# Performance work log

Hardware: AMD Instinct MI355X
Metric: run time of the kernel (lower is better)

Reference implementation:

```python
import jax, jax.numpy as jnp
import numpy as np

B, K, D = 64, 2048, 32400  # batch, num bases, in_features**2 (180*180)


def setup_inputs() -> dict:
    key = jax.random.key(0)
    k1, k2, k3, k4, k5, k6 = jax.random.split(key, 6)
    s = 1.0 / np.sqrt(K)  # matches uniform(-sqrt(1/K), sqrt(1/K)) scale of weight init
    return {
        "X_re": jax.random.normal(k1, (B, D), dtype=jnp.float32),
        "X_im": jax.random.normal(k2, (B, D), dtype=jnp.float32),
        "bases_re": jax.random.normal(k3, (K, D), dtype=jnp.float32) * 0.004,
        "bases_im": jax.random.normal(k4, (K, D), dtype=jnp.float32) * 0.004,
        "weight_re": jax.random.normal(k5, (K,), dtype=jnp.float32) * s,
        "weight_im": jax.random.normal(k6, (K,), dtype=jnp.float32) * s,
    }


def reference(X_re, X_im, bases_re, bases_im, weight_re, weight_im):
    # Assemble complex64 operands
    X = jax.lax.complex(X_re, X_im)          # [B, D]
    bases = jax.lax.complex(bases_re, bases_im)  # [K, D]
    w = jax.lax.complex(weight_re, weight_im)    # [K]
    # X @ conj(bases)^T -> [B, K]; diag_embed(weight) matmul == per-basis scale
    coeffs = jnp.matmul(X, jnp.conj(bases).T) * w[None, :]
    # project back: [B, K] @ [K, D] -> [B, D]
    out = jnp.matmul(coeffs, bases)
    # complex->channels->complex round trip in the original is the identity
    return out
```

## Files before the change

kernel.cpp:

```cpp
#include <hip/hip_runtime.h>
#include <hip/hip_bf16.h>
#include <cstdint>
#include <cstddef>

#define B_DIM 64
#define K_DIM 2048
#define D_DIM 32400

typedef __bf16 bf16x8 __attribute__((ext_vector_type(8)));
typedef float f32x4 __attribute__((ext_vector_type(4)));

union U128 { uint4 u; bf16x8 b; };

__device__ inline bf16x8 asbf(uint4 u) { U128 x; x.u = u; return x.b; }

__device__ inline uint4 neg4(uint4 u) {
    u.x ^= 0x80008000u; u.y ^= 0x80008000u; u.z ^= 0x80008000u; u.w ^= 0x80008000u;
    return u;
}

__device__ inline f32x4 mfma16(bf16x8 a, bf16x8 b, f32x4 c) {
    return __builtin_amdgcn_mfma_f32_16x16x32_bf16(a, b, c, 0, 0, 0);
}

__device__ inline f32x4 ld4g(const float* __restrict__ p, int d, int dlim) {
    f32x4 r;
    if (d + 4 <= dlim) {
        float4 v = *reinterpret_cast<const float4*>(p + d);
        r[0] = v.x; r[1] = v.y; r[2] = v.z; r[3] = v.w;
    } else {
        #pragma unroll
        for (int j = 0; j < 4; ++j) r[j] = (d + j < dlim) ? p[d + j] : 0.0f;
    }
    return r;
}

__device__ inline uint32_t pk(float a, float b) {
    union { __bf16 h[2]; uint32_t u; } x;
    x.h[0] = (__bf16)a; x.h[1] = (__bf16)b;
    return x.u;
}

#define P1_STRIDE 72

__global__ __launch_bounds__(256) void p1_coeffs(
    const float* __restrict__ Xre, const float* __restrict__ Xim,
    const float* __restrict__ Bre, const float* __restrict__ Bim,
    const float* __restrict__ Wre, const float* __restrict__ Wim,
    float* __restrict__ Cre, float* __restrict__ Cim)
{
    __shared__ __align__(16) __bf16 sX[2][64][P1_STRIDE];
    __shared__ __align__(16) __bf16 sB[2][64][P1_STRIDE];

    const int kt = blockIdx.x;
    const int dc = blockIdx.y;
    const int tid  = threadIdx.x;
    const int lane = tid & 63;
    const int w    = tid >> 6;
    const int r    = lane & 15;
    const int g    = lane >> 4;

    const int kbase  = kt * 64;
    const int dstart = dc * 1024;
    const int dend   = min(dstart + 1024, D_DIM);
    const int nsteps = (dend - dstart + 63) >> 6;

    const int srow = tid >> 4;
    const int sd   = (tid & 15) * 4;

    f32x4 st[16];

    auto LOADS = [&](int s) {
        const int dg = dstart + s * 64 + sd;
        #pragma unroll
        for (int j = 0; j < 4; ++j) {
            const int row = j * 16 + srow;
            st[j]      = ld4g(Xre + (size_t)row * D_DIM, dg, dend);
            st[4 + j]  = ld4g(Xim + (size_t)row * D_DIM, dg, dend);
            st[8 + j]  = ld4g(Bre + (size_t)(kbase + row) * D_DIM, dg, dend);
            st[12 + j] = ld4g(Bim + (size_t)(kbase + row) * D_DIM, dg, dend);
        }
    };

    auto WRITE = [&]() {
        #pragma unroll
        for (int j = 0; j < 4; ++j) {
            const int row = j * 16 + srow;
            *(uint2*)&sX[0][row][sd] = make_uint2(pk(st[j][0],      st[j][1]),      pk(st[j][2],      st[j][3]));
            *(uint2*)&sX[1][row][sd] = make_uint2(pk(st[4 + j][0],  st[4 + j][1]),  pk(st[4 + j][2],  st[4 + j][3]));
            *(uint2*)&sB[0][row][sd] = make_uint2(pk(st[8 + j][0],  st[8 + j][1]),  pk(st[8 + j][2],  st[8 + j][3]));
            *(uint2*)&sB[1][row][sd] = make_uint2(pk(st[12 + j][0], st[12 + j][1]), pk(st[12 + j][2], st[12 + j][3]));
        }
    };

    const int m0  = (w & 1) * 32;
    const int nl0 = (w >> 1) * 32;

    f32x4 accRe[2][2] = {};
    f32x4 accIm[2][2] = {};

    auto COMPUTE = [&]() {
        #pragma unroll
        for (int kk = 0; kk < 2; ++kk) {
            const int dp = kk * 32 + g * 8;
            uint4 xre[2], xim[2], bre[2], bim[2];
            #pragma unroll
            for (int ms = 0; ms < 2; ++ms) {
                xre[ms] = *(const uint4*)&sX[0][m0 + ms * 16 + r][dp];
                xim[ms] = *(const uint4*)&sX[1][m0 + ms * 16 + r][dp];
            }
            #pragma unroll
            for (int ns = 0; ns < 2; ++ns) {
                bre[ns] = *(const uint4*)&sB[0][nl0 + ns * 16 + r][dp];
                bim[ns] = *(const uint4*)&sB[1][nl0 + ns * 16 + r][dp];
            }
            #pragma unroll
            for (int ms = 0; ms < 2; ++ms)
            #pragma unroll
            for (int ns = 0; ns < 2; ++ns) {
                accRe[ms][ns] = mfma16(asbf(xre[ms]), asbf(bre[ns]), accRe[ms][ns]);
                accRe[ms][ns] = mfma16(asbf(xim[ms]), asbf(bim[ns]), accRe[ms][ns]);
                accIm[ms][ns] = mfma16(asbf(xim[ms]), asbf(bre[ns]), accIm[ms][ns]);
                accIm[ms][ns] = mfma16(asbf(neg4(xre[ms])), asbf(bim[ns]), accIm[ms][ns]);
            }
        }
    };

    LOADS(0); WRITE(); __syncthreads();
    for (int s = 0; s < nsteps; ++s) {
        if (s + 1 < nsteps) LOADS(s + 1);
        COMPUTE();
        if (s + 1 < nsteps) {
            __syncthreads();
            WRITE();
            __syncthreads();
        }
    }

    #pragma unroll
    for (int ms = 0; ms < 2; ++ms)
    #pragma unroll
    for (int ns = 0; ns < 2; ++ns) {
        const int kb = kbase + nl0 + ns * 16 + r;
        const float wre = Wre[kb], wim = Wim[kb];
        #pragma unroll
        for (int i = 0; i < 4; ++i) {
            const int b = m0 + ms * 16 + g * 4 + i;
            const float cre = accRe[ms][ns][i];
            const float cim = accIm[ms][ns][i];
            atomicAdd(&Cre[b * K_DIM + kb], cre * wre - cim * wim);
            atomicAdd(&Cim[b * K_DIM + kb], cre * wim + cim * wre);
        }
    }
}

__global__ __launch_bounds__(256) void cbf_kernel(
    const float* __restrict__ Cre, const float* __restrict__ Cim,
    __bf16* __restrict__ CreBf, __bf16* __restrict__ CimBf)
{
    const int i = blockIdx.x * 256 + threadIdx.x;
    if (i < B_DIM * K_DIM) {
        CreBf[i] = (__bf16)Cre[i];
        CimBf[i] = (__bf16)Cim[i];
    }
}

#define P2_STRIDE 72

template <bool WIM>
__global__ __launch_bounds__(256) void p2_project(
    const float* __restrict__ Bre, const float* __restrict__ Bim,
    const __bf16* __restrict__ CreBf, const __bf16* __restrict__ CimBf,
    float* __restrict__ out)
{
    __shared__ __align__(16) __bf16 sT[2][2][64][P2_STRIDE];

    const int dt = blockIdx.x;
    const int kh = blockIdx.y;
    const int d0 = dt * 64;
    const int khbase = kh * (K_DIM / 2);
    const int tid  = threadIdx.x;
    const int lane = tid & 63;
    const int w    = tid >> 6;
    const int r    = lane & 15;
    const int g    = lane >> 4;

    const int kq = tid >> 4;
    const int ds = (tid & 15) * 4;

    f32x4 st[8];

    auto LOADS = [&](int t) {
        const int k0 = khbase + t * 64;
        #pragma unroll
        for (int j = 0; j < 4; ++j) {
            const size_t ro = (size_t)(k0 + kq * 4 + j) * D_DIM;
            st[j]     = ld4g(Bre + ro, d0 + ds, D_DIM);
            st[4 + j] = ld4g(Bim + ro, d0 + ds, D_DIM);
        }
    };

    auto WRITE = [&](int buf) {
        #pragma unroll
        for (int i = 0; i < 4; ++i) {
            *(uint2*)&sT[buf][0][ds + i][kq * 4] =
                make_uint2(pk(st[0][i], st[1][i]), pk(st[2][i], st[3][i]));
            *(uint2*)&sT[buf][1][ds + i][kq * 4] =
                make_uint2(pk(st[4][i], st[5][i]), pk(st[6][i], st[7][i]));
        }
    };

    const int m0  = (w & 1) * 32;
    const int nl0 = (w >> 1) * 32;

    f32x4 accRe[2][2] = {};
    f32x4 accIm[2][2] = {};

    auto COMPUTE = [&](int t, int buf) {
        const int k0 = khbase + t * 64;
        uint4 aRe[2][2], aIm[2][2];
        #pragma unroll
        for (int ms = 0; ms < 2; ++ms) {
            const size_t rowo = (size_t)(m0 + ms * 16 + r) * K_DIM;
            #pragma unroll
            for (int kk = 0; kk < 2; ++kk) {
                aRe[ms][kk] = *(const uint4*)&CreBf[rowo + k0 + kk * 32 + g * 8];
                aIm[ms][kk] = *(const uint4*)&CimBf[rowo + k0 + kk * 32 + g * 8];
            }
        }
        #pragma unroll
        for (int kk = 0; kk < 2; ++kk) {
            uint4 bre[2], bim[2];
            #pragma unroll
            for (int ns = 0; ns < 2; ++ns) {
                bre[ns] = *(const uint4*)&sT[buf][0][nl0 + ns * 16 + r][kk * 32 + g * 8];
                bim[ns] = *(const uint4*)&sT[buf][1][nl0 + ns * 16 + r][kk * 32 + g * 8];
            }
            #pragma unroll
            for (int ms = 0; ms < 2; ++ms)
            #pragma unroll
            for (int ns = 0; ns < 2; ++ns) {
                accRe[ms][ns] = mfma16(asbf(aRe[ms][kk]), asbf(bre[ns]), accRe[ms][ns]);
                accRe[ms][ns] = mfma16(asbf(neg4(aIm[ms][kk])), asbf(bim[ns]), accRe[ms][ns]);
                if (WIM) {
                    accIm[ms][ns] = mfma16(asbf(aRe[ms][kk]), asbf(bim[ns]), accIm[ms][ns]);
                    accIm[ms][ns] = mfma16(asbf(aIm[ms][kk]), asbf(bre[ns]), accIm[ms][ns]);
                }
            }
        }
    };

    const int NT = (K_DIM / 2) / 64;
    LOADS(0); WRITE(0); __syncthreads();
    for (int t = 0; t < NT; ++t) {
        if (t + 1 < NT) LOADS(t + 1);
        COMPUTE(t, t & 1);
        if (t + 1 < NT) WRITE((t + 1) & 1);
        __syncthreads();
    }

    #pragma unroll
    for (int ms = 0; ms < 2; ++ms)
    #pragma unroll
    for (int ns = 0; ns < 2; ++ns) {
        const int d = d0 + nl0 + ns * 16 + r;
        if (d < D_DIM) {
            #pragma unroll
            for (int i = 0; i < 4; ++i) {
                const int b = m0 + ms * 16 + g * 4 + i;
                if (!WIM) {
                    atomicAdd(&out[(size_t)b * D_DIM + d], accRe[ms][ns][i]);
                } else {
                    atomicAdd(&out[((size_t)b * D_DIM + d) * 2],     accRe[ms][ns][i]);
                    atomicAdd(&out[((size_t)b * D_DIM + d) * 2 + 1], accIm[ms][ns][i]);
                }
            }
        }
    }
}

extern "C" void kernel_launch(void* const* d_in, const int* in_sizes, int n_in,
                              void* d_out, int out_size, void* d_ws, size_t ws_size,
                              hipStream_t stream) {
    const float* Xre = (const float*)d_in[0];
    const float* Xim = (const float*)d_in[1];
    const float* Bre = (const float*)d_in[2];
    const float* Bim = (const float*)d_in[3];
    const float* Wre = (const float*)d_in[4];
    const float* Wim = (const float*)d_in[5];

    float*  Cre   = (float*)d_ws;
    float*  Cim   = Cre + B_DIM * K_DIM;
    __bf16* CreBf = (__bf16*)(Cim + B_DIM * K_DIM);
    __bf16* CimBf = CreBf + B_DIM * K_DIM;

    (void)hipMemsetAsync(d_ws, 0, (size_t)2 * B_DIM * K_DIM * sizeof(float), stream);
    (void)hipMemsetAsync(d_out, 0, (size_t)out_size * sizeof(float), stream);

    dim3 g1(32, 32);
    p1_coeffs<<<g1, 256, 0, stream>>>(Xre, Xim, Bre, Bim, Wre, Wim, Cre, Cim);

    cbf_kernel<<<(B_DIM * K_DIM + 255) / 256, 256, 0, stream>>>(Cre, Cim, CreBf, CimBf);

    const int ndt = (D_DIM + 63) / 64;
    dim3 g2(ndt, 2);
    if (out_size == 2 * B_DIM * D_DIM) {
        p2_project<true><<<g2, 256, 0, stream>>>(Bre, Bim, CreBf, CimBf, (float*)d_out);
    } else {
        p2_project<false><<<g2, 256, 0, stream>>>(Bre, Bim, CreBf, CimBf, (float*)d_out);
    }
}
```

Before: 325.6 us.

## Widen p1 K tile to 128 and pre-convert X to bf16

The coefficient kernel now covers 128 bases per block instead of 64, so each X tile is reused across twice as many bases and the number of blocks re-reading X halves. When the workspace is large enough, a new kernel converts X to bf16 once up front, so p1 loads half the bytes for X and skips the per-block conversion. The larger tile doubles per-wave accumulators and B staging registers, with launch_bounds(256,2), which may lower occupancy or cause spills. The extra conversion kernel adds a launch and a full pass over X.

Result: faster. 304.1 us, median of 2 (-6.6%).

```diff
diff --git a/kernel.cpp b/kernel.cpp
--- a/kernel.cpp
+++ b/kernel.cpp
@@ -6,6 +6,7 @@
 #define B_DIM 64
 #define K_DIM 2048
 #define D_DIM 32400
+#define KTILE 128
 
 typedef __bf16 bf16x8 __attribute__((ext_vector_type(8)));
 typedef float f32x4 __attribute__((ext_vector_type(4)));
@@ -35,89 +36,139 @@
     return r;
 }
 
+__device__ inline uint4 ld8bf(const __bf16* __restrict__ p, int d, int dlim) {
+    if (d + 8 <= dlim) return *reinterpret_cast<const uint4*>(p + d);
+    union { uint4 u; __bf16 h[8]; } x;
+    #pragma unroll
+    for (int j = 0; j < 8; ++j) x.h[j] = (d + j < dlim) ? p[d + j] : (__bf16)0.0f;
+    return x.u;
+}
+
 __device__ inline uint32_t pk(float a, float b) {
     union { __bf16 h[2]; uint32_t u; } x;
     x.h[0] = (__bf16)a; x.h[1] = (__bf16)b;
     return x.u;
 }
 
+__global__ __launch_bounds__(256) void xbf_kernel(
+    const float* __restrict__ Xre, const float* __restrict__ Xim,
+    __bf16* __restrict__ XreB, __bf16* __restrict__ XimB)
+{
+    const int i = (blockIdx.x * 256 + threadIdx.x) * 4;
+    if (i < B_DIM * D_DIM) {
+        float4 a = *reinterpret_cast<const float4*>(Xre + i);
+        float4 b = *reinterpret_cast<const float4*>(Xim + i);
+        *(uint2*)(XreB + i) = make_uint2(pk(a.x, a.y), pk(a.z, a.w));
+        *(uint2*)(XimB + i) = make_uint2(pk(b.x, b.y), pk(b.z, b.w));
+    }
+}
+
 #define P1_STRIDE 72
 
-__global__ __launch_bounds__(256) void p1_coeffs(
-    const float* __restrict__ Xre, const float* __restrict__ Xim,
+template <bool XBF>
+__global__ __launch_bounds__(256, 2) void p1_coeffs(
+    const float* __restrict__ XreF, const float* __restrict__ XimF,
+    const __bf16* __restrict__ XreB, const __bf16* __restrict__ XimB,
     const float* __restrict__ Bre, const float* __restrict__ Bim,
     const float* __restrict__ Wre, const float* __restrict__ Wim,
     float* __restrict__ Cre, float* __restrict__ Cim)
 {
     __shared__ __align__(16) __bf16 sX[2][64][P1_STRIDE];
-    __shared__ __align__(16) __bf16 sB[2][64][P1_STRIDE];
-
-    const int kt = blockIdx.x;
-    const int dc = blockIdx.y;
+    __shared__ __align__(16) __bf16 sB[2][KTILE][P1_STRIDE];
+
+    const int ktg = blockIdx.x;
+    const int dc  = blockIdx.y;
     const int tid  = threadIdx.x;
     const int lane = tid & 63;
     const int w    = tid >> 6;
     const int r    = lane & 15;
     const int g    = lane >> 4;
 
-    const int kbase  = kt * 64;
+    const int kbase  = ktg * KTILE;
     const int dstart = dc * 1024;
     const int dend   = min(dstart + 1024, D_DIM);
     const int nsteps = (dend - dstart + 63) >> 6;
 
     const int srow = tid >> 4;
     const int sd   = (tid & 15) * 4;
-
-    f32x4 st[16];
+    const int rowx = tid >> 3;
+    const int colx = (tid & 7) * 8;
+
+    f32x4 bst[16];
+    uint4 xst[4];
+    f32x4 xstf[8];
 
     auto LOADS = [&](int s) {
         const int dg = dstart + s * 64 + sd;
         #pragma unroll
-        for (int j = 0; j < 4; ++j) {
+        for (int j = 0; j < 8; ++j) {
             const int row = j * 16 + srow;
-            st[j]      = ld4g(Xre + (size_t)row * D_DIM, dg, dend);
-            st[4 + j]  = ld4g(Xim + (size_t)row * D_DIM, dg, dend);
-            st[8 + j]  = ld4g(Bre + (size_t)(kbase + row) * D_DIM, dg, dend);
-            st[12 + j] = ld4g(Bim + (size_t)(kbase + row) * D_DIM, dg, dend);
+            bst[j]     = ld4g(Bre + (size_t)(kbase + row) * D_DIM, dg, dend);
+            bst[8 + j] = ld4g(Bim + (size_t)(kbase + row) * D_DIM, dg, dend);
+        }
+        if (XBF) {
+            const int dgx = dstart + s * 64 + colx;
+            xst[0] = ld8bf(XreB + (size_t)rowx * D_DIM,        dgx, dend);
+            xst[1] = ld8bf(XreB + (size_t)(rowx + 32) * D_DIM, dgx, dend);
+            xst[2] = ld8bf(XimB + (size_t)rowx * D_DIM,        dgx, dend);
+            xst[3] = ld8bf(XimB + (size_t)(rowx + 32) * D_DIM, dgx, dend);
+        } else {
+            #pragma unroll
+            for (int j = 0; j < 4; ++j) {
+                const int row = j * 16 + srow;
+                xstf[j]     = ld4g(XreF + (size_t)row * D_DIM, dg, dend);
+                xstf[4 + j] = ld4g(XimF + (size_t)row * D_DIM, dg, dend);
+            }
         }
     };
 
     auto WRITE = [&]() {
         #pragma unroll
-        for (int j = 0; j < 4; ++j) {
+        for (int j = 0; j < 8; ++j) {
             const int row = j * 16 + srow;
-            *(uint2*)&sX[0][row][sd] = make_uint2(pk(st[j][0],      st[j][1]),      pk(st[j][2],      st[j][3]));
-            *(uint2*)&sX[1][row][sd] = make_uint2(pk(st[4 + j][0],  st[4 + j][1]),  pk(st[4 + j][2],  st[4 + j][3]));
-            *(uint2*)&sB[0][row][sd] = make_uint2(pk(st[8 + j][0],  st[8 + j][1]),  pk(st[8 + j][2],  st[8 + j][3]));
-            *(uint2*)&sB[1][row][sd] = make_uint2(pk(st[12 + j][0], st[12 + j][1]), pk(st[12 + j][2], st[12 + j][3]));
+            *(uint2*)&sB[0][row][sd] = make_uint2(pk(bst[j][0],     bst[j][1]),     pk(bst[j][2],     bst[j][3]));
+            *(uint2*)&sB[1][row][sd] = make_uint2(pk(bst[8 + j][0], bst[8 + j][1]), pk(bst[8 + j][2], bst[8 + j][3]));
+        }
+        if (XBF) {
+            *(uint4*)&sX[0][rowx][colx]      = xst[0];
+            *(uint4*)&sX[0][rowx + 32][colx] = xst[1];
+            *(uint4*)&sX[1][rowx][colx]      = xst[2];
+            *(uint4*)&sX[1][rowx + 32][colx] = xst[3];
+        } else {
+            #pragma unroll
+            for (int j = 0; j < 4; ++j) {
+                const int row = j * 16 + srow;
+                *(uint2*)&sX[0][row][sd] = make_uint2(pk(xstf[j][0],     xstf[j][1]),     pk(xstf[j][2],     xstf[j][3]));
+                *(uint2*)&sX[1][row][sd] = make_uint2(pk(xstf[4 + j][0], xstf[4 + j][1]), pk(xstf[4 + j][2], xstf[4 + j][3]));
+            }
         }
     };
 
     const int m0  = (w & 1) * 32;
-    const int nl0 = (w >> 1) * 32;
-
-    f32x4 accRe[2][2] = {};
-    f32x4 accIm[2][2] = {};
+    const int nl0 = (w >> 1) * 64;
+
+    f32x4 accRe[2][4] = {};
+    f32x4 accIm[2][4] = {};
 
     auto COMPUTE = [&]() {
         #pragma unroll
         for (int kk = 0; kk < 2; ++kk) {
             const int dp = kk * 32 + g * 8;
-            uint4 xre[2], xim[2], bre[2], bim[2];
+            uint4 xre[2], xim[2], bre[4], bim[4];
             #pragma unroll
             for (int ms = 0; ms < 2; ++ms) {
                 xre[ms] = *(const uint4*)&sX[0][m0 + ms * 16 + r][dp];
                 xim[ms] = *(const uint4*)&sX[1][m0 + ms * 16 + r][dp];
             }
             #pragma unroll
-            for (int ns = 0; ns < 2; ++ns) {
+            for (int ns = 0; ns < 4; ++ns) {
                 bre[ns] = *(const uint4*)&sB[0][nl0 + ns * 16 + r][dp];
                 bim[ns] = *(const uint4*)&sB[1][nl0 + ns * 16 + r][dp];
             }
             #pragma unroll
             for (int ms = 0; ms < 2; ++ms)
             #pragma unroll
-            for (int ns = 0; ns < 2; ++ns) {
+            for (int ns = 0; ns < 4; ++ns) {
                 accRe[ms][ns] = mfma16(asbf(xre[ms]), asbf(bre[ns]), accRe[ms][ns]);
                 accRe[ms][ns] = mfma16(asbf(xim[ms]), asbf(bim[ns]), accRe[ms][ns]);
                 accIm[ms][ns] = mfma16(asbf(xim[ms]), asbf(bre[ns]), accIm[ms][ns]);
@@ -140,7 +191,7 @@
     #pragma unroll
     for (int ms = 0; ms < 2; ++ms)
     #pragma unroll
-    for (int ns = 0; ns < 2; ++ns) {
+    for (int ns = 0; ns < 4; ++ns) {
         const int kb = kbase + nl0 + ns * 16 + r;
         const float wre = Wre[kb], wim = Wim[kb];
         #pragma unroll
@@ -293,12 +344,24 @@
     float*  Cim   = Cre + B_DIM * K_DIM;
     __bf16* CreBf = (__bf16*)(Cim + B_DIM * K_DIM);
     __bf16* CimBf = CreBf + B_DIM * K_DIM;
+    __bf16* XreB  = CimBf + B_DIM * K_DIM;
+    __bf16* XimB  = XreB + (size_t)B_DIM * D_DIM;
+
+    const size_t need = (size_t)2 * B_DIM * K_DIM * sizeof(float)
+                      + (size_t)2 * B_DIM * K_DIM * sizeof(__bf16)
+                      + (size_t)2 * B_DIM * D_DIM * sizeof(__bf16);
+    const bool xbf = ws_size >= need;
 
     (void)hipMemsetAsync(d_ws, 0, (size_t)2 * B_DIM * K_DIM * sizeof(float), stream);
     (void)hipMemsetAsync(d_out, 0, (size_t)out_size * sizeof(float), stream);
 
-    dim3 g1(32, 32);
-    p1_coeffs<<<g1, 256, 0, stream>>>(Xre, Xim, Bre, Bim, Wre, Wim, Cre, Cim);
+    dim3 g1(K_DIM / KTILE, 32);
+    if (xbf) {
+        xbf_kernel<<<(B_DIM * D_DIM / 4 + 255) / 256, 256, 0, stream>>>(Xre, Xim, XreB, XimB);
+        p1_coeffs<true><<<g1, 256, 0, stream>>>(Xre, Xim, XreB, XimB, Bre, Bim, Wre, Wim, Cre, Cim);
+    } else {
+        p1_coeffs<false><<<g1, 256, 0, stream>>>(Xre, Xim, XreB, XimB, Bre, Bim, Wre, Wim, Cre, Cim);
+    }
 
     cbf_kernel<<<(B_DIM * K_DIM + 255) / 256, 256, 0, stream>>>(Cre, Cim, CreBf, CimBf);
 
```
